# Optimization experiments

Measured on AMD Instinct MI355X. Metric: run time of the kernel, lower is better.

Reference implementation:

```python
import jax, jax.numpy as jnp
import numpy as np

B, H, W, N, DIM = 2, 64, 64, 4, 128
HEADS = 4
SPLIT = 2          # split_size; idx == 0 -> window = (H, SPLIT)
HEAD_DIM = DIM // HEADS
SCALE = HEAD_DIM ** -0.5


def setup_inputs() -> dict:
    key = jax.random.key(0)
    k1, k2, k3, k4 = jax.random.split(key, 4)
    query = jax.random.normal(k1, (B, H, W, N, DIM), jnp.float32)
    key_t = jax.random.normal(k2, (B, H, W, N, DIM), jnp.float32)
    value = jax.random.normal(k3, (B, H, W, N, DIM), jnp.float32)
    conv_w = jax.random.normal(k4, (DIM, 1, 3, 3), jnp.float32) * 0.1  # depthwise get_v
    return {"query": query, "key": key_t, "value": value, "conv_w": conv_w}


def _im2cswin(x, hs, ws, heads):
    # b (i hs) (j ws) n (h d) -> (b i j) h (hs ws n) d
    b, ht, wd, n, c = x.shape
    i, j = ht // hs, wd // ws
    d = c // heads
    x = x.reshape(b, i, hs, j, ws, n, heads, d)
    x = x.transpose(0, 1, 3, 6, 2, 4, 5, 7)  # b i j h hs ws n d
    return x.reshape(b * i * j, heads, hs * ws * n, d)


def _cswin_forward(query, key, value, conv_w):
    b, ht, wd, n, c = query.shape
    hs, ws = ht, SPLIT  # idx == 0; ht % hs == 0 and wd % ws == 0 -> no padding
    i, j = ht // hs, wd // ws
    Bw = b * i * j

    q = _im2cswin(query, hs, ws, HEADS) * SCALE
    k = _im2cswin(key, hs, ws, HEADS)

    # --- get_rpe (locally-enhanced positional encoding on value) ---
    # value windows: b i j n c hs ws
    vw = value.reshape(b, i, hs, j, ws, n, c).transpose(0, 1, 3, 5, 6, 2, 4)
    vw = vw.reshape(Bw, n, c, hs, ws)
    vimg = vw.reshape(Bw * n, c, hs, ws)
    conv = jax.lax.conv_general_dilated(
        vimg, conv_w, window_strides=(1, 1), padding=((1, 1), (1, 1)),
        dimension_numbers=("NCHW", "OIHW", "NCHW"), feature_group_count=c)
    conv = conv.reshape(Bw, n, c, hs, ws)
    rpe = conv.sum(axis=1, keepdims=True)  # Bw 1 c hs ws
    # subtract center-tap contribution of all other candidates at same pixel
    mask_n = (1.0 - jnp.eye(n, dtype=query.dtype)) * -1.0  # (n, n)
    center = conv_w[:, 0, 1, 1]  # (c,)
    tmp = vw * center[None, None, :, None, None]
    tmp = jnp.einsum("jk,bkdhw->bjdhw", mask_n, tmp)
    rpe = rpe + tmp  # Bw n c hs ws

    def to_tokens(t):
        # b n (h d) hs ws -> b h (hs ws n) d
        t = t.reshape(Bw, n, HEADS, HEAD_DIM, hs, ws)
        t = t.transpose(0, 2, 4, 5, 1, 3)
        return t.reshape(Bw, HEADS, hs * ws * n, HEAD_DIM)

    rpe = to_tokens(rpe)
    v = to_tokens(vw)

    # --- window attention mask: block self-edges between candidates at same pixel ---
    L = hs * ws * n
    tok = jnp.arange(L)
    sp = tok // n  # spatial index of each token
    amask = jnp.where(sp[:, None] == sp[None, :], -jnp.inf, 0.0)
    amask = jnp.where(tok[:, None] == tok[None, :], 0.0, amask).astype(query.dtype)

    attn = jnp.einsum("bhic,bhjc->bhij", q, k) + amask[None, None]
    attn = jax.nn.softmax(attn, axis=-1)
    x = jnp.einsum("bhij,bhjc->bhic", attn, v) + rpe

    # (b i j) h (hs ws n) d -> b (i hs) (j ws) n (h d)
    x = x.reshape(b, i, j, HEADS, hs, ws, n, HEAD_DIM)
    x = x.transpose(0, 1, 4, 2, 5, 6, 3, 7).reshape(b, ht, wd, n, c)
    return x


def reference(query, key, value, conv_w):
    return _cswin_forward(query, key, value, conv_w)
```

## Files before the change

kernel.cpp:

```cpp
#include <hip/hip_runtime.h>
#include <stdint.h>


typedef __bf16 bf16x8 __attribute__((ext_vector_type(8)));
typedef float f32x4 __attribute__((ext_vector_type(4)));
typedef float f32x2 __attribute__((ext_vector_type(2)));

#if __has_builtin(__builtin_amdgcn_exp2f)
#define EXP2F __builtin_amdgcn_exp2f
#else
#define EXP2F exp2f
#endif

union U4 { uint4 u; bf16x8 v; unsigned short s[8]; };

__device__ __forceinline__ float bf2f(unsigned short h){ union{unsigned u;float f;}x; x.u=((unsigned)h)<<16; return x.f; }

__device__ __forceinline__ unsigned cvtpk(float lo, float hi){
  unsigned d;
  asm("v_cvt_pk_bf16_f32 %0, %1, %2" : "=v"(d) : "v"(lo), "v"(hi));
  return d;
}
__device__ __forceinline__ U4 pack8(float4 a, float4 b){
  U4 r;
  r.u.x = cvtpk(a.x, a.y); r.u.y = cvtpk(a.z, a.w);
  r.u.z = cvtpk(b.x, b.y); r.u.w = cvtpk(b.z, b.w);
  return r;
}

__device__ __forceinline__ void pls32(unsigned &a, unsigned &b){
#if __has_builtin(__builtin_amdgcn_permlane32_swap)
  auto r = __builtin_amdgcn_permlane32_swap(a, b, false, false);
  a = r[0]; b = r[1];
#else
  unsigned sa_ = __shfl_xor(a, 32), sb_ = __shfl_xor(b, 32);
  bool hi = ((threadIdx.x & 32) != 0);
  unsigned na = hi ? sb_ : a, nb = hi ? b : sa_;
  a = na; b = nb;
#endif
}
__device__ __forceinline__ void pls16(unsigned &a, unsigned &b){
#if __has_builtin(__builtin_amdgcn_permlane16_swap)
  auto r = __builtin_amdgcn_permlane16_swap(a, b, false, false);
  a = r[0]; b = r[1];
#else
  unsigned sa_ = __shfl_xor(a, 16), sb_ = __shfl_xor(b, 16);
  bool hi = ((threadIdx.x & 16) != 0);
  unsigned na = hi ? sb_ : a, nb = hi ? b : sa_;
  a = na; b = nb;
#endif
}

__device__ __forceinline__ void xpose_p(const unsigned w[4][2], U4& ap0, U4& ap1)
{
  unsigned a0 = w[0][0], b0 = w[1][0]; pls32(a0, b0); pls16(a0, b0);
  unsigned a1 = w[0][1], b1 = w[1][1]; pls32(a1, b1); pls16(a1, b1);
  ap0.u.x = a0; ap0.u.y = a1; ap0.u.z = b0; ap0.u.w = b1;
  unsigned c0 = w[2][0], d0 = w[3][0]; pls32(c0, d0); pls16(c0, d0);
  unsigned c1 = w[2][1], d1 = w[3][1]; pls32(c1, d1); pls16(c1, d1);
  ap1.u.x = c0; ap1.u.y = c1; ap1.u.z = d0; ap1.u.w = d1;
}

#define C_SCALE 0.25506953149031837f
#define M_SHIFT 20.0f

__device__ __forceinline__ void sm_pack(const f32x4* s, unsigned w[4][2], f32x2& l2)
{
  const f32x2 m2 = {-M_SHIFT, -M_SHIFT};
#pragma unroll
  for (int t = 0; t < 4; t++){
    f32x2 x0 = {s[t][0], s[t][1]};
    f32x2 x1 = {s[t][2], s[t][3]};
    f32x2 y0 = x0 * C_SCALE + m2;
    f32x2 y1 = x1 * C_SCALE + m2;
    float p0 = EXP2F(y0.x), p1 = EXP2F(y0.y);
    float p2 = EXP2F(y1.x), p3 = EXP2F(y1.y);
    l2 += (f32x2){p0, p1};
    l2 += (f32x2){p2, p3};
    w[t][0] = cvtpk(p0, p1);
    w[t][1] = cvtpk(p2, p3);
  }
}

#define VT_OFF 0
#define LDS_BYTES 32768

__global__ __launch_bounds__(256, 4) void cswin_attn_kernel(
    const float* __restrict__ qg,
    const float* __restrict__ kg,
    const float* __restrict__ vg,
    const float* __restrict__ cwg,
    float* __restrict__ outg)
{
  __shared__ __align__(16) unsigned char smem[LDS_BYTES];
  const int tid = threadIdx.x;
  const int lane = tid & 63;
  const int wave = tid >> 6;
  const int qd = lane >> 4;
  const int n  = lane & 15;

  const int swn = (n & 7) << 2;
  const int xb0 = ((4 * qd) ^ swn) << 2;
  const int xb1 = xb0 ^ 64;

  const int bh = blockIdx.x & 255;
  const int q4 = blockIdx.x >> 8;
  const int head = bh & 3;
  const int bw = bh >> 2;
  const int b  = bw >> 5;
  const int jj = bw & 31;

  const size_t wbase = (size_t)b * 2097152 + (size_t)(jj * 2) * 512 + head * 32;

  {
    int l0 = tid * 2;
    size_t off = wbase + (size_t)(l0 >> 3) * 32768 + (size_t)((l0 >> 2) & 1) * 512 + (l0 & 3) * 128;
    const float* p0 = vg + off;
    float v0[32], v1[32];
#pragma unroll
    for (int c = 0; c < 8; c++){
      float4 a = ((const float4*)p0)[c];
      v0[c*4+0]=a.x; v0[c*4+1]=a.y; v0[c*4+2]=a.z; v0[c*4+3]=a.w;
    }
#pragma unroll
    for (int c = 0; c < 8; c++){
      float4 a = ((const float4*)(p0 + 128))[c];
      v1[c*4+0]=a.x; v1[c*4+1]=a.y; v1[c*4+2]=a.z; v1[c*4+3]=a.w;
    }
#pragma unroll
    for (int d = 0; d < 32; d++)
      *(unsigned*)(smem + VT_OFF + d * 1024 + ((tid ^ ((d & 7) << 2)) << 2)) =
          cvtpk(v0[d], v1[d]);
  }
  __syncthreads();

  const size_t lane_base = wbase + (size_t)(n >> 3) * 32768 + (size_t)((n >> 2) & 1) * 512 +
                           (size_t)(n & 3) * 128 + qd * 8;

  const int row0  = q4 * 128 + wave * 32;
  const int tilea = row0 >> 4;
  const int cka   = tilea >> 2;
  const int ta    = tilea & 3;

  U4 bqa, bqb;
  {
    const float* qa = qg + lane_base + (size_t)tilea * 65536;
    const float* qb = qa + 65536;
    bqa = pack8(((const float4*)qa)[0], ((const float4*)qa)[1]);
    bqb = pack8(((const float4*)qb)[0], ((const float4*)qb)[1]);
  }

  f32x4 o0a={0,0,0,0}, o1a={0,0,0,0}, o0b={0,0,0,0}, o1b={0,0,0,0};
  f32x2 la2 = {0.f,0.f}, lb2 = {0.f,0.f};

  float4 nxt[8];
#pragma unroll
  for (int t = 0; t < 4; t++){
    const float* kp = kg + lane_base + (size_t)t * 65536;
    nxt[2*t] = ((const float4*)kp)[0]; nxt[2*t+1] = ((const float4*)kp)[1];
  }

#pragma unroll 1
  for (int ck = 0; ck < 8; ck++){
    U4 ak[4];
#pragma unroll
    for (int t = 0; t < 4; t++) ak[t] = pack8(nxt[2*t], nxt[2*t+1]);
    if (ck < 7){
#pragma unroll
      for (int t = 0; t < 4; t++){
        const float* kp = kg + lane_base + (size_t)((ck + 1) * 4 + t) * 65536;
        nxt[2*t] = ((const float4*)kp)[0]; nxt[2*t+1] = ((const float4*)kp)[1];
      }
    }

    const f32x4 zero = {0.f,0.f,0.f,0.f};
    f32x4 sa[4], sb[4];
#pragma unroll
    for (int t = 0; t < 4; t++){
      sa[t] = __builtin_amdgcn_mfma_f32_16x16x32_bf16(ak[t].v, bqa.v, zero, 0, 0, 0);
      sb[t] = __builtin_amdgcn_mfma_f32_16x16x32_bf16(ak[t].v, bqb.v, zero, 0, 0, 0);
    }
    if (ck == cka){
      bool dq = (qd == (n >> 2));
#pragma unroll
      for (int r = 0; r < 4; r++)
        if (dq && r != (n & 3)){ sa[ta][r] = -1e30f; sb[ta+1][r] = -1e30f; }
    }

    unsigned wA[4][2], wB[4][2];
    sm_pack(sa, wA, la2);
    sm_pack(sb, wB, lb2);

    const unsigned char* vr0 = smem + VT_OFF + n * 1024 + ck * 128;
    const unsigned char* vr1 = vr0 + 16 * 1024;
    U4 bv00, bv01, bv10, bv11;
    bv00.u = *(const uint4*)(vr0 + xb0);
    bv01.u = *(const uint4*)(vr0 + xb1);
    bv10.u = *(const uint4*)(vr1 + xb0);
    bv11.u = *(const uint4*)(vr1 + xb1);

    U4 apA0, apA1, apB0, apB1;
    xpose_p(wA, apA0, apA1);
    xpose_p(wB, apB0, apB1);

    o0a = __builtin_amdgcn_mfma_f32_16x16x32_bf16(apA0.v, bv00.v, o0a, 0, 0, 0);
    o0a = __builtin_amdgcn_mfma_f32_16x16x32_bf16(apA1.v, bv01.v, o0a, 0, 0, 0);
    o1a = __builtin_amdgcn_mfma_f32_16x16x32_bf16(apA0.v, bv10.v, o1a, 0, 0, 0);
    o1a = __builtin_amdgcn_mfma_f32_16x16x32_bf16(apA1.v, bv11.v, o1a, 0, 0, 0);
    o0b = __builtin_amdgcn_mfma_f32_16x16x32_bf16(apB0.v, bv00.v, o0b, 0, 0, 0);
    o0b = __builtin_amdgcn_mfma_f32_16x16x32_bf16(apB1.v, bv01.v, o0b, 0, 0, 0);
    o1b = __builtin_amdgcn_mfma_f32_16x16x32_bf16(apB0.v, bv10.v, o1b, 0, 0, 0);
    o1b = __builtin_amdgcn_mfma_f32_16x16x32_bf16(apB1.v, bv11.v, o1b, 0, 0, 0);
  }

  float w9[2][9];
#pragma unroll
  for (int nt = 0; nt < 2; nt++){
    int c = head * 32 + nt * 16 + n;
#pragma unroll
    for (int t9 = 0; t9 < 9; t9++) w9[nt][t9] = cwg[c * 9 + t9];
  }

  float la = la2.x + la2.y, lb = lb2.x + lb2.y;
  la += __shfl_xor(la, 16); la += __shfl_xor(la, 32);
  lb += __shfl_xor(lb, 16); lb += __shfl_xor(lb, 32);

  const float ila = 1.f / la, ilb = 1.f / lb;

#pragma unroll
  for (int mt = 0; mt < 2; mt++){
    const int m0 = row0 + mt * 16;
    const float ilv = mt ? ilb : ila;
    const f32x4 oo0 = mt ? o0b : o0a;
    const f32x4 oo1 = mt ? o1b : o1a;
    float il[4];
#pragma unroll
    for (int r = 0; r < 4; r++) il[r] = __shfl(ilv, qd * 4 + r);

    const int sp = (m0 >> 2) + qd;
    const int h_ = sp >> 1, w_ = sp & 1;

    float accs[2], cw2[2], vfs[2][4];
#pragma unroll
    for (int nt = 0; nt < 2; nt++){
      const int d = nt * 16 + n;
      const unsigned char* VTd = smem + VT_OFF + d * 1024;
      float acc = 0.f;
#pragma unroll
      for (int dy = -1; dy <= 1; dy++){
        int h2 = h_ + dy;
        bool hv = (h2 >= 0) && (h2 <= 63);
        int h2c = hv ? h2 : h_;
#pragma unroll
        for (int wp = 0; wp < 2; wp++){
          bool valid = hv && !((dy == 0) && (wp == w_));
          int ti = (dy + 1) * 3 + 1 + wp - w_;
          int spn = h2c * 2 + wp;
          uint2 sv = *(const uint2*)(VTd + (((2 * spn) ^ swn) << 2));
          float s = bf2f((unsigned short)(sv.x & 0xffff)) + bf2f((unsigned short)(sv.x >> 16))
                  + bf2f((unsigned short)(sv.y & 0xffff)) + bf2f((unsigned short)(sv.y >> 16));
          acc += (valid ? w9[nt][ti] : 0.f) * s;
        }
      }
      accs[nt] = acc;
      cw2[nt] = w9[nt][4];
      uint2 vv4 = *(const uint2*)(VTd + ((((m0 >> 1) + 2 * qd) ^ swn) << 2));
      vfs[nt][0] = bf2f((unsigned short)(vv4.x & 0xffff));
      vfs[nt][1] = bf2f((unsigned short)(vv4.x >> 16));
      vfs[nt][2] = bf2f((unsigned short)(vv4.y & 0xffff));
      vfs[nt][3] = bf2f((unsigned short)(vv4.y >> 16));
    }

    const size_t obase = (size_t)b * 2097152 + (size_t)h_ * 32768 +
                         (size_t)(jj * 2 + w_) * 512 + head * 32;
#pragma unroll
    for (int r = 0; r < 4; r++){
      float r0 = oo0[r] * il[r] + accs[0] + cw2[0] * vfs[0][r];
      float r1 = oo1[r] * il[r] + accs[1] + cw2[1] * vfs[1][r];
      outg[obase + (size_t)r * 128 + n]      = r0;
      outg[obase + (size_t)r * 128 + 16 + n] = r1;
    }
  }
}

extern "C" void kernel_launch(void* const* d_in, const int* in_sizes, int n_in,
                              void* d_out, int out_size, void* d_ws, size_t ws_size,
                              hipStream_t stream) {
  (void)in_sizes; (void)n_in; (void)d_ws; (void)ws_size; (void)out_size;
  cswin_attn_kernel<<<dim3(1024), dim3(256), 0, stream>>>(
      (const float*)d_in[0], (const float*)d_in[1], (const float*)d_in[2],
      (const float*)d_in[3], (float*)d_out);
}
```

Before: 134.7 us.

## Give each wave one query tile and process keys in half-size chunks

Blocks grow from 4 to 8 waves, and each wave now handles a single 16-row query tile instead of two. The K loop now walks 16 chunks of 32 keys instead of 8 chunks of 64, which shrinks live register state and lets more waves hide latency. Block indices are remapped so that neighbouring blocks share head windows, which may improve L2 reuse, and the Q/K prefetch is issued before the barrier so it overlaps the V staging. In exchange, each wave re-reads K per query tile, so K traffic per useful MFMA doubles, and each wave runs more loop iterations with less independent work.

```diff
diff --git a/kernel.cpp b/kernel.cpp
--- a/kernel.cpp
+++ b/kernel.cpp
@@ -4,7 +4,6 @@
 
 typedef __bf16 bf16x8 __attribute__((ext_vector_type(8)));
 typedef float f32x4 __attribute__((ext_vector_type(4)));
-typedef float f32x2 __attribute__((ext_vector_type(2)));
 
 #if __has_builtin(__builtin_amdgcn_exp2f)
 #define EXP2F __builtin_amdgcn_exp2f
@@ -51,41 +50,13 @@
 #endif
 }
 
-__device__ __forceinline__ void xpose_p(const unsigned w[4][2], U4& ap0, U4& ap1)
-{
-  unsigned a0 = w[0][0], b0 = w[1][0]; pls32(a0, b0); pls16(a0, b0);
-  unsigned a1 = w[0][1], b1 = w[1][1]; pls32(a1, b1); pls16(a1, b1);
-  ap0.u.x = a0; ap0.u.y = a1; ap0.u.z = b0; ap0.u.w = b1;
-  unsigned c0 = w[2][0], d0 = w[3][0]; pls32(c0, d0); pls16(c0, d0);
-  unsigned c1 = w[2][1], d1 = w[3][1]; pls32(c1, d1); pls16(c1, d1);
-  ap1.u.x = c0; ap1.u.y = c1; ap1.u.z = d0; ap1.u.w = d1;
-}
-
 #define C_SCALE 0.25506953149031837f
 #define M_SHIFT 20.0f
 
-__device__ __forceinline__ void sm_pack(const f32x4* s, unsigned w[4][2], f32x2& l2)
-{
-  const f32x2 m2 = {-M_SHIFT, -M_SHIFT};
-#pragma unroll
-  for (int t = 0; t < 4; t++){
-    f32x2 x0 = {s[t][0], s[t][1]};
-    f32x2 x1 = {s[t][2], s[t][3]};
-    f32x2 y0 = x0 * C_SCALE + m2;
-    f32x2 y1 = x1 * C_SCALE + m2;
-    float p0 = EXP2F(y0.x), p1 = EXP2F(y0.y);
-    float p2 = EXP2F(y1.x), p3 = EXP2F(y1.y);
-    l2 += (f32x2){p0, p1};
-    l2 += (f32x2){p2, p3};
-    w[t][0] = cvtpk(p0, p1);
-    w[t][1] = cvtpk(p2, p3);
-  }
-}
-
 #define VT_OFF 0
 #define LDS_BYTES 32768
 
-__global__ __launch_bounds__(256, 4) void cswin_attn_kernel(
+__global__ __launch_bounds__(512, 8) void cswin_attn_kernel(
     const float* __restrict__ qg,
     const float* __restrict__ kg,
     const float* __restrict__ vg,
@@ -100,19 +71,25 @@
   const int n  = lane & 15;
 
   const int swn = (n & 7) << 2;
-  const int xb0 = ((4 * qd) ^ swn) << 2;
-  const int xb1 = xb0 ^ 64;
-
-  const int bh = blockIdx.x & 255;
-  const int q4 = blockIdx.x >> 8;
+
+  const int bid = blockIdx.x;
+  const int bh = ((bid >> 5) << 3) | (bid & 7);
+  const int q4 = (bid >> 3) & 3;
   const int head = bh & 3;
   const int bw = bh >> 2;
   const int b  = bw >> 5;
   const int jj = bw & 31;
 
   const size_t wbase = (size_t)b * 2097152 + (size_t)(jj * 2) * 512 + head * 32;
-
-  {
+  const size_t lane_base = wbase + (size_t)(n >> 3) * 32768 + (size_t)((n >> 2) & 1) * 512 +
+                           (size_t)(n & 3) * 128 + qd * 8;
+
+  const int row0  = q4 * 128 + wave * 16;
+  const int tilea = row0 >> 4;
+  const int cka2  = tilea >> 1;
+  const int ta2   = tilea & 1;
+
+  if (tid < 256){
     int l0 = tid * 2;
     size_t off = wbase + (size_t)(l0 >> 3) * 32768 + (size_t)((l0 >> 2) & 1) * 512 + (l0 & 3) * 128;
     const float* p0 = vg + off;
@@ -132,85 +109,79 @@
       *(unsigned*)(smem + VT_OFF + d * 1024 + ((tid ^ ((d & 7) << 2)) << 2)) =
           cvtpk(v0[d], v1[d]);
   }
-  __syncthreads();
-
-  const size_t lane_base = wbase + (size_t)(n >> 3) * 32768 + (size_t)((n >> 2) & 1) * 512 +
-                           (size_t)(n & 3) * 128 + qd * 8;
-
-  const int row0  = q4 * 128 + wave * 32;
-  const int tilea = row0 >> 4;
-  const int cka   = tilea >> 2;
-  const int ta    = tilea & 3;
-
-  U4 bqa, bqb;
+
+  float4 qr0, qr1;
   {
     const float* qa = qg + lane_base + (size_t)tilea * 65536;
-    const float* qb = qa + 65536;
-    bqa = pack8(((const float4*)qa)[0], ((const float4*)qa)[1]);
-    bqb = pack8(((const float4*)qb)[0], ((const float4*)qb)[1]);
-  }
-
-  f32x4 o0a={0,0,0,0}, o1a={0,0,0,0}, o0b={0,0,0,0}, o1b={0,0,0,0};
-  f32x2 la2 = {0.f,0.f}, lb2 = {0.f,0.f};
-
-  float4 nxt[8];
-#pragma unroll
-  for (int t = 0; t < 4; t++){
-    const float* kp = kg + lane_base + (size_t)t * 65536;
-    nxt[2*t] = ((const float4*)kp)[0]; nxt[2*t+1] = ((const float4*)kp)[1];
-  }
+    qr0 = ((const float4*)qa)[0]; qr1 = ((const float4*)qa)[1];
+  }
+  float4 n0, n1, n2, n3;
+  {
+    const float* kp0 = kg + lane_base;
+    const float* kp1 = kg + lane_base + 65536;
+    n0 = ((const float4*)kp0)[0]; n1 = ((const float4*)kp0)[1];
+    n2 = ((const float4*)kp1)[0]; n3 = ((const float4*)kp1)[1];
+  }
+
+  __syncthreads();
+
+  U4 bq = pack8(qr0, qr1);
+
+  f32x4 o0={0,0,0,0}, o1={0,0,0,0};
+  float la = 0.f;
 
 #pragma unroll 1
-  for (int ck = 0; ck < 8; ck++){
-    U4 ak[4];
-#pragma unroll
-    for (int t = 0; t < 4; t++) ak[t] = pack8(nxt[2*t], nxt[2*t+1]);
-    if (ck < 7){
-#pragma unroll
-      for (int t = 0; t < 4; t++){
-        const float* kp = kg + lane_base + (size_t)((ck + 1) * 4 + t) * 65536;
-        nxt[2*t] = ((const float4*)kp)[0]; nxt[2*t+1] = ((const float4*)kp)[1];
+  for (int ck2 = 0; ck2 < 16; ck2++){
+    U4 ak0 = pack8(n0, n1);
+    U4 ak1 = pack8(n2, n3);
+    if (ck2 < 15){
+      const float* kp0 = kg + lane_base + (size_t)(2 * ck2 + 2) * 65536;
+      const float* kp1 = kg + lane_base + (size_t)(2 * ck2 + 3) * 65536;
+      n0 = ((const float4*)kp0)[0]; n1 = ((const float4*)kp0)[1];
+      n2 = ((const float4*)kp1)[0]; n3 = ((const float4*)kp1)[1];
+    }
+
+    const f32x4 zero = {0.f,0.f,0.f,0.f};
+    f32x4 sa0 = __builtin_amdgcn_mfma_f32_16x16x32_bf16(ak0.v, bq.v, zero, 0, 0, 0);
+    f32x4 sa1 = __builtin_amdgcn_mfma_f32_16x16x32_bf16(ak1.v, bq.v, zero, 0, 0, 0);
+
+    if (ck2 == cka2){
+      bool dq = (qd == (n >> 2));
+      if (ta2 == 0){
+#pragma unroll
+        for (int r = 0; r < 4; r++) if (dq && r != (n & 3)) sa0[r] = -1e30f;
+      } else {
+#pragma unroll
+        for (int r = 0; r < 4; r++) if (dq && r != (n & 3)) sa1[r] = -1e30f;
       }
     }
 
-    const f32x4 zero = {0.f,0.f,0.f,0.f};
-    f32x4 sa[4], sb[4];
-#pragma unroll
-    for (int t = 0; t < 4; t++){
-      sa[t] = __builtin_amdgcn_mfma_f32_16x16x32_bf16(ak[t].v, bqa.v, zero, 0, 0, 0);
-      sb[t] = __builtin_amdgcn_mfma_f32_16x16x32_bf16(ak[t].v, bqb.v, zero, 0, 0, 0);
-    }
-    if (ck == cka){
-      bool dq = (qd == (n >> 2));
-#pragma unroll
-      for (int r = 0; r < 4; r++)
-        if (dq && r != (n & 3)){ sa[ta][r] = -1e30f; sb[ta+1][r] = -1e30f; }
-    }
-
-    unsigned wA[4][2], wB[4][2];
-    sm_pack(sa, wA, la2);
-    sm_pack(sb, wB, lb2);
-
-    const unsigned char* vr0 = smem + VT_OFF + n * 1024 + ck * 128;
+    const int idx = ck2 * 16 + 4 * qd;
+    const int xb = ((idx ^ swn) << 2);
+    const unsigned char* vr0 = smem + VT_OFF + n * 1024 + xb;
     const unsigned char* vr1 = vr0 + 16 * 1024;
-    U4 bv00, bv01, bv10, bv11;
-    bv00.u = *(const uint4*)(vr0 + xb0);
-    bv01.u = *(const uint4*)(vr0 + xb1);
-    bv10.u = *(const uint4*)(vr1 + xb0);
-    bv11.u = *(const uint4*)(vr1 + xb1);
-
-    U4 apA0, apA1, apB0, apB1;
-    xpose_p(wA, apA0, apA1);
-    xpose_p(wB, apB0, apB1);
-
-    o0a = __builtin_amdgcn_mfma_f32_16x16x32_bf16(apA0.v, bv00.v, o0a, 0, 0, 0);
-    o0a = __builtin_amdgcn_mfma_f32_16x16x32_bf16(apA1.v, bv01.v, o0a, 0, 0, 0);
-    o1a = __builtin_amdgcn_mfma_f32_16x16x32_bf16(apA0.v, bv10.v, o1a, 0, 0, 0);
-    o1a = __builtin_amdgcn_mfma_f32_16x16x32_bf16(apA1.v, bv11.v, o1a, 0, 0, 0);
-    o0b = __builtin_amdgcn_mfma_f32_16x16x32_bf16(apB0.v, bv00.v, o0b, 0, 0, 0);
-    o0b = __builtin_amdgcn_mfma_f32_16x16x32_bf16(apB1.v, bv01.v, o0b, 0, 0, 0);
-    o1b = __builtin_amdgcn_mfma_f32_16x16x32_bf16(apB0.v, bv10.v, o1b, 0, 0, 0);
-    o1b = __builtin_amdgcn_mfma_f32_16x16x32_bf16(apB1.v, bv11.v, o1b, 0, 0, 0);
+    U4 bv0, bv1;
+    bv0.u = *(const uint4*)vr0;
+    bv1.u = *(const uint4*)vr1;
+
+    float p00 = EXP2F(__builtin_fmaf(sa0[0], C_SCALE, -M_SHIFT));
+    float p01 = EXP2F(__builtin_fmaf(sa0[1], C_SCALE, -M_SHIFT));
+    float p02 = EXP2F(__builtin_fmaf(sa0[2], C_SCALE, -M_SHIFT));
+    float p03 = EXP2F(__builtin_fmaf(sa0[3], C_SCALE, -M_SHIFT));
+    float p10 = EXP2F(__builtin_fmaf(sa1[0], C_SCALE, -M_SHIFT));
+    float p11 = EXP2F(__builtin_fmaf(sa1[1], C_SCALE, -M_SHIFT));
+    float p12 = EXP2F(__builtin_fmaf(sa1[2], C_SCALE, -M_SHIFT));
+    float p13 = EXP2F(__builtin_fmaf(sa1[3], C_SCALE, -M_SHIFT));
+    la += ((p00 + p01) + (p02 + p03)) + ((p10 + p11) + (p12 + p13));
+    unsigned w00 = cvtpk(p00, p01), w01 = cvtpk(p02, p03);
+    unsigned w10 = cvtpk(p10, p11), w11 = cvtpk(p12, p13);
+
+    unsigned a0 = w00, b0 = w10; pls32(a0, b0); pls16(a0, b0);
+    unsigned a1 = w01, b1 = w11; pls32(a1, b1); pls16(a1, b1);
+    U4 pa; pa.u.x = a0; pa.u.y = a1; pa.u.z = b0; pa.u.w = b1;
+
+    o0 = __builtin_amdgcn_mfma_f32_16x16x32_bf16(pa.v, bv0.v, o0, 0, 0, 0);
+    o1 = __builtin_amdgcn_mfma_f32_16x16x32_bf16(pa.v, bv1.v, o1, 0, 0, 0);
   }
 
   float w9[2][9];
@@ -221,21 +192,14 @@
     for (int t9 = 0; t9 < 9; t9++) w9[nt][t9] = cwg[c * 9 + t9];
   }
 
-  float la = la2.x + la2.y, lb = lb2.x + lb2.y;
   la += __shfl_xor(la, 16); la += __shfl_xor(la, 32);
-  lb += __shfl_xor(lb, 16); lb += __shfl_xor(lb, 32);
-
-  const float ila = 1.f / la, ilb = 1.f / lb;
-
-#pragma unroll
-  for (int mt = 0; mt < 2; mt++){
-    const int m0 = row0 + mt * 16;
-    const float ilv = mt ? ilb : ila;
-    const f32x4 oo0 = mt ? o0b : o0a;
-    const f32x4 oo1 = mt ? o1b : o1a;
+  const float ila = 1.f / la;
+
+  {
+    const int m0 = row0;
     float il[4];
 #pragma unroll
-    for (int r = 0; r < 4; r++) il[r] = __shfl(ilv, qd * 4 + r);
+    for (int r = 0; r < 4; r++) il[r] = __shfl(ila, qd * 4 + r);
 
     const int sp = (m0 >> 2) + qd;
     const int h_ = sp >> 1, w_ = sp & 1;
@@ -275,8 +239,8 @@
                          (size_t)(jj * 2 + w_) * 512 + head * 32;
 #pragma unroll
     for (int r = 0; r < 4; r++){
-      float r0 = oo0[r] * il[r] + accs[0] + cw2[0] * vfs[0][r];
-      float r1 = oo1[r] * il[r] + accs[1] + cw2[1] * vfs[1][r];
+      float r0 = o0[r] * il[r] + accs[0] + cw2[0] * vfs[0][r];
+      float r1 = o1[r] * il[r] + accs[1] + cw2[1] * vfs[1][r];
       outg[obase + (size_t)r * 128 + n]      = r0;
       outg[obase + (size_t)r * 128 + 16 + n] = r1;
     }
@@ -287,7 +251,7 @@
                               void* d_out, int out_size, void* d_ws, size_t ws_size,
                               hipStream_t stream) {
   (void)in_sizes; (void)n_in; (void)d_ws; (void)ws_size; (void)out_size;
-  cswin_attn_kernel<<<dim3(1024), dim3(256), 0, stream>>>(
+  cswin_attn_kernel<<<dim3(1024), dim3(512), 0, stream>>>(
       (const float*)d_in[0], (const float*)d_in[1], (const float*)d_in[2],
       (const float*)d_in[3], (float*)d_out);
 }
```

New measurement: 166.8 us. +23.9%, slower.

## Stage K into LDS cooperatively and remap block order for L2 locality

Applied to the files above, without the earlier changes.

K is now loaded once per block cooperatively, converted to bf16 and stored in a swizzled LDS region, replacing the per-lane streaming of K from global memory with register prefetch. The V staging is rewritten to use coalesced float4 loads with scattered 16-bit transposed LDS stores. The block index mapping is changed so that blocks sharing the same window and head run close together in time. LDS doubles to 64 KB and launch bounds drop to 2 blocks per SM, which lowers occupancy, and the byte-granular LDS stores may cause bank conflicts.

```diff
diff --git a/kernel.cpp b/kernel.cpp
--- a/kernel.cpp
+++ b/kernel.cpp
@@ -64,28 +64,11 @@
 #define C_SCALE 0.25506953149031837f
 #define M_SHIFT 20.0f
 
-__device__ __forceinline__ void sm_pack(const f32x4* s, unsigned w[4][2], f32x2& l2)
-{
-  const f32x2 m2 = {-M_SHIFT, -M_SHIFT};
-#pragma unroll
-  for (int t = 0; t < 4; t++){
-    f32x2 x0 = {s[t][0], s[t][1]};
-    f32x2 x1 = {s[t][2], s[t][3]};
-    f32x2 y0 = x0 * C_SCALE + m2;
-    f32x2 y1 = x1 * C_SCALE + m2;
-    float p0 = EXP2F(y0.x), p1 = EXP2F(y0.y);
-    float p2 = EXP2F(y1.x), p3 = EXP2F(y1.y);
-    l2 += (f32x2){p0, p1};
-    l2 += (f32x2){p2, p3};
-    w[t][0] = cvtpk(p0, p1);
-    w[t][1] = cvtpk(p2, p3);
-  }
-}
-
 #define VT_OFF 0
-#define LDS_BYTES 32768
-
-__global__ __launch_bounds__(256, 4) void cswin_attn_kernel(
+#define KS_OFF 32768
+#define LDS_BYTES 65536
+
+__global__ __launch_bounds__(256, 2) void cswin_attn_kernel(
     const float* __restrict__ qg,
     const float* __restrict__ kg,
     const float* __restrict__ vg,
@@ -103,37 +86,15 @@
   const int xb0 = ((4 * qd) ^ swn) << 2;
   const int xb1 = xb0 ^ 64;
 
-  const int bh = blockIdx.x & 255;
-  const int q4 = blockIdx.x >> 8;
+  const int bid = blockIdx.x;
+  const int bh = ((bid >> 5) << 3) | (bid & 7);
+  const int q4 = (bid >> 3) & 3;
   const int head = bh & 3;
   const int bw = bh >> 2;
   const int b  = bw >> 5;
   const int jj = bw & 31;
 
   const size_t wbase = (size_t)b * 2097152 + (size_t)(jj * 2) * 512 + head * 32;
-
-  {
-    int l0 = tid * 2;
-    size_t off = wbase + (size_t)(l0 >> 3) * 32768 + (size_t)((l0 >> 2) & 1) * 512 + (l0 & 3) * 128;
-    const float* p0 = vg + off;
-    float v0[32], v1[32];
-#pragma unroll
-    for (int c = 0; c < 8; c++){
-      float4 a = ((const float4*)p0)[c];
-      v0[c*4+0]=a.x; v0[c*4+1]=a.y; v0[c*4+2]=a.z; v0[c*4+3]=a.w;
-    }
-#pragma unroll
-    for (int c = 0; c < 8; c++){
-      float4 a = ((const float4*)(p0 + 128))[c];
-      v1[c*4+0]=a.x; v1[c*4+1]=a.y; v1[c*4+2]=a.z; v1[c*4+3]=a.w;
-    }
-#pragma unroll
-    for (int d = 0; d < 32; d++)
-      *(unsigned*)(smem + VT_OFF + d * 1024 + ((tid ^ ((d & 7) << 2)) << 2)) =
-          cvtpk(v0[d], v1[d]);
-  }
-  __syncthreads();
-
   const size_t lane_base = wbase + (size_t)(n >> 3) * 32768 + (size_t)((n >> 2) & 1) * 512 +
                            (size_t)(n & 3) * 128 + qd * 8;
 
@@ -142,36 +103,65 @@
   const int cka   = tilea >> 2;
   const int ta    = tilea & 3;
 
-  U4 bqa, bqb;
+  float4 qra0, qra1, qrb0, qrb1;
   {
     const float* qa = qg + lane_base + (size_t)tilea * 65536;
     const float* qb = qa + 65536;
-    bqa = pack8(((const float4*)qa)[0], ((const float4*)qa)[1]);
-    bqb = pack8(((const float4*)qb)[0], ((const float4*)qb)[1]);
-  }
+    qra0 = ((const float4*)qa)[0]; qra1 = ((const float4*)qa)[1];
+    qrb0 = ((const float4*)qb)[0]; qrb1 = ((const float4*)qb)[1];
+  }
+
+  {
+    const int tk = tid >> 3;
+    const int p  = tid & 7;
+#pragma unroll 1
+    for (int rr = 0; rr < 2; rr++){
+      float4 va[8], ka[8];
+#pragma unroll
+      for (int r = 0; r < 8; r++){
+        int T = (rr * 8 + r) * 32 + tk;
+        size_t toff = wbase + (size_t)(T >> 3) * 32768 + (size_t)((T >> 2) & 1) * 512 +
+                      (size_t)(T & 3) * 128 + p * 4;
+        va[r] = *(const float4*)(vg + toff);
+        ka[r] = *(const float4*)(kg + toff);
+      }
+#pragma unroll
+      for (int r = 0; r < 8; r++){
+        int T = (rr * 8 + r) * 32 + tk;
+        unsigned short h0 = (unsigned short)cvtpk(va[r].x, va[r].x);
+        unsigned short h1 = (unsigned short)cvtpk(va[r].y, va[r].y);
+        unsigned short h2 = (unsigned short)cvtpk(va[r].z, va[r].z);
+        unsigned short h3 = (unsigned short)cvtpk(va[r].w, va[r].w);
+        int R0 = 4 * p;
+        *(unsigned short*)(smem + VT_OFF + (R0+0) * 1024 + ((T*2) ^ (((R0+0)&7)<<4))) = h0;
+        *(unsigned short*)(smem + VT_OFF + (R0+1) * 1024 + ((T*2) ^ (((R0+1)&7)<<4))) = h1;
+        *(unsigned short*)(smem + VT_OFF + (R0+2) * 1024 + ((T*2) ^ (((R0+2)&7)<<4))) = h2;
+        *(unsigned short*)(smem + VT_OFF + (R0+3) * 1024 + ((T*2) ^ (((R0+3)&7)<<4))) = h3;
+        uint2 kw; kw.x = cvtpk(ka[r].x, ka[r].y); kw.y = cvtpk(ka[r].z, ka[r].w);
+        *(uint2*)(smem + KS_OFF + T * 64 + ((p*8) ^ ((T&3)<<4))) = kw;
+      }
+    }
+  }
+
+  __syncthreads();
+
+  U4 bqa = pack8(qra0, qra1);
+  U4 bqb = pack8(qrb0, qrb1);
 
   f32x4 o0a={0,0,0,0}, o1a={0,0,0,0}, o0b={0,0,0,0}, o1b={0,0,0,0};
   f32x2 la2 = {0.f,0.f}, lb2 = {0.f,0.f};
 
-  float4 nxt[8];
-#pragma unroll
-  for (int t = 0; t < 4; t++){
-    const float* kp = kg + lane_base + (size_t)t * 65536;
-    nxt[2*t] = ((const float4*)kp)[0]; nxt[2*t+1] = ((const float4*)kp)[1];
-  }
+  const int kxb = (qd * 16) ^ ((n & 3) << 4);
+  const unsigned char* kbase = smem + KS_OFF + n * 64 + kxb;
 
 #pragma unroll 1
   for (int ck = 0; ck < 8; ck++){
     U4 ak[4];
-#pragma unroll
-    for (int t = 0; t < 4; t++) ak[t] = pack8(nxt[2*t], nxt[2*t+1]);
-    if (ck < 7){
-#pragma unroll
-      for (int t = 0; t < 4; t++){
-        const float* kp = kg + lane_base + (size_t)((ck + 1) * 4 + t) * 65536;
-        nxt[2*t] = ((const float4*)kp)[0]; nxt[2*t+1] = ((const float4*)kp)[1];
-      }
-    }
+    const unsigned char* kb = kbase + ck * 4096;
+    ak[0].u = *(const uint4*)(kb);
+    ak[1].u = *(const uint4*)(kb + 1024);
+    ak[2].u = *(const uint4*)(kb + 2048);
+    ak[3].u = *(const uint4*)(kb + 3072);
 
     const f32x4 zero = {0.f,0.f,0.f,0.f};
     f32x4 sa[4], sb[4];
@@ -188,8 +178,27 @@
     }
 
     unsigned wA[4][2], wB[4][2];
-    sm_pack(sa, wA, la2);
-    sm_pack(sb, wB, lb2);
+    {
+      const f32x2 m2 = {-M_SHIFT, -M_SHIFT};
+#pragma unroll
+      for (int t = 0; t < 4; t++){
+        f32x2 y0 = (f32x2){sa[t][0], sa[t][1]} * C_SCALE + m2;
+        f32x2 y1 = (f32x2){sa[t][2], sa[t][3]} * C_SCALE + m2;
+        float p0 = EXP2F(y0.x), p1 = EXP2F(y0.y);
+        float p2 = EXP2F(y1.x), p3 = EXP2F(y1.y);
+        la2 += (f32x2){p0, p1}; la2 += (f32x2){p2, p3};
+        wA[t][0] = cvtpk(p0, p1); wA[t][1] = cvtpk(p2, p3);
+      }
+#pragma unroll
+      for (int t = 0; t < 4; t++){
+        f32x2 y0 = (f32x2){sb[t][0], sb[t][1]} * C_SCALE + m2;
+        f32x2 y1 = (f32x2){sb[t][2], sb[t][3]} * C_SCALE + m2;
+        float p0 = EXP2F(y0.x), p1 = EXP2F(y0.y);
+        float p2 = EXP2F(y1.x), p3 = EXP2F(y1.y);
+        lb2 += (f32x2){p0, p1}; lb2 += (f32x2){p2, p3};
+        wB[t][0] = cvtpk(p0, p1); wB[t][1] = cvtpk(p2, p3);
+      }
+    }
 
     const unsigned char* vr0 = smem + VT_OFF + n * 1024 + ck * 128;
     const unsigned char* vr1 = vr0 + 16 * 1024;
```

Measured after the change: 117.9 us. -12.5%, faster.
